# Kernel optimization log

Hardware: AMD Instinct MI355X
Metric: run time of the kernel (lower is better)

The kernel has to match this reference:

```python
import jax, jax.numpy as jnp
import numpy as np

BS = 64; T = 96; C = 16; IN = 16; H = 256; NH = 8; DH = H // NH
NCLS = 4; L = T + NCLS; LAYERS = 4; GDEP = 2; EPS = 1e-5


def _ln(x, g, b):
    m = x.mean(-1, keepdims=True)
    v = ((x - m) ** 2).mean(-1, keepdims=True)
    return (x - m) / jnp.sqrt(v + EPS) * g + b


def _mask():
    # causal upper-triangular -inf mask; last NCLS rows (cls tokens) attend everywhere
    m = jnp.where(jnp.triu(jnp.ones((L, L), jnp.float32), 1) > 0, -jnp.inf, 0.0)
    return m.at[-NCLS:].set(0.0)


def _enc(h, mask, Wqkv, bqkv, Wo, bo, W1, b1, W2, b2, g1, be1, g2, be2):
    # post-norm TransformerEncoderLayer (torch default), dropout=0
    B = h.shape[0]
    qkv = h @ Wqkv.T + bqkv
    q, k, v = jnp.split(qkv, 3, axis=-1)
    sp = lambda t: t.reshape(B, L, NH, DH).transpose(0, 2, 1, 3)
    q, k, v = sp(q), sp(k), sp(v)
    s = jnp.einsum('bhqd,bhkd->bhqk', q, k) / np.float32(np.sqrt(DH)) + mask
    a = jax.nn.softmax(s, axis=-1)
    o = jnp.einsum('bhqk,bhkd->bhqd', a, v).transpose(0, 2, 1, 3).reshape(B, L, H)
    h = _ln(h + o @ Wo.T + bo, g1, be1)
    ff = jax.nn.relu(h @ W1.T + b1) @ W2.T + b2
    return _ln(h + ff, g2, be2)


def _mixprop(x, g, Wm, bm):
    # x: (bs, H, C, NCLS); MTGNN mixprop with alpha=0
    adj = g + jnp.eye(C, dtype=g.dtype)
    a = adj / adj.sum(1, keepdims=True)
    h = x
    outs = [x]
    for _ in range(GDEP):
        h = jnp.einsum('ncwl,vw->ncvl', h, a)
        outs.append(h)
    ho = jnp.concatenate(outs, axis=1)  # (bs, (GDEP+1)*H, C, NCLS)
    return jnp.einsum('ncwl,oc->nowl', ho, Wm) + bm[None, :, None, None]


def _forward(x, Wfc, bfc, cls_token, pos_emb, emb1, emb2, Wl1, bl1, Wl2, bl2,
             Wqkv, bqkv, Wo, bo, W1, b1, W2, b2, ln1g, ln1b, ln2g, ln2b,
             Wmlp, bmlp, Wd1, bd1, Wd2, bd2):
    bs = x.shape[0]
    h = x @ Wfc.T + bfc                                      # (bs,T,C,H)
    h = jnp.concatenate([h, jnp.broadcast_to(cls_token, (bs, NCLS, C, H))], axis=1)
    h = h + pos_emb[None]                                    # (bs,L,C,H)
    h = jnp.swapaxes(h, 1, 2).reshape(bs * C, L, H)
    mask = _mask()
    # graph_constructor (alpha=1)
    m1 = jnp.tanh(emb1 @ Wl1.T + bl1)
    m2 = jnp.tanh(emb2 @ Wl2.T + bl2)
    g = jax.nn.relu(jnp.tanh(m1 @ m2.T - m2 @ m1.T))         # (C,C)
    h = _enc(h, mask, Wqkv[0], bqkv[0], Wo[0], bo[0], W1[0], b1[0], W2[0], b2[0],
             ln1g[0], ln1b[0], ln2g[0], ln2b[0])
    for l in range(1, LAYERS):
        cls = h[:, -NCLS:].reshape(bs, C, NCLS, H).transpose(0, 3, 1, 2)  # (bs,H,C,NCLS)
        cls = _mixprop(cls, g, Wmlp[l - 1], bmlp[l - 1])
        cls = cls.transpose(0, 2, 3, 1).reshape(bs * C, NCLS, H)
        h = jnp.concatenate([h[:, :-NCLS], cls], axis=1)
        h = _enc(h, mask, Wqkv[l], bqkv[l], Wo[l], bo[l], W1[l], b1[l], W2[l], b2[l],
                 ln1g[l], ln1b[l], ln2g[l], ln2b[l])
    z = jnp.tanh(h[:, -NCLS:].reshape(bs, C * NCLS * H))
    z = jax.nn.gelu(z @ Wd1.T + bd1, approximate=False) @ Wd2.T + bd2
    return z[:, 0]


def setup_inputs() -> dict:
    key = jax.random.key(0)
    ks = iter(jax.random.split(key, 64))
    rn = lambda *s: jax.random.normal(next(ks), s, dtype=jnp.float32) * 0.05
    d = {}
    d['x'] = jax.random.normal(next(ks), (BS, T, C, IN), dtype=jnp.float32)
    d['p'] = jnp.zeros((BS,), jnp.float32)
    d['y'] = jnp.zeros((BS,), jnp.float32)
    d['Wfc'] = rn(H, IN); d['bfc'] = jnp.zeros((H,), jnp.float32)
    d['cls_token'] = rn(1, NCLS, C, H) * 20.0  # torch randn scale ~1
    d['pos_emb'] = rn(NCLS + T, C, H) * 20.0
    d['emb1'] = rn(C, H); d['emb2'] = rn(C, H)
    d['Wl1'] = rn(H, H); d['bl1'] = jnp.zeros((H,), jnp.float32)
    d['Wl2'] = rn(H, H); d['bl2'] = jnp.zeros((H,), jnp.float32)
    d['Wqkv'] = rn(LAYERS, 3 * H, H); d['bqkv'] = jnp.zeros((LAYERS, 3 * H), jnp.float32)
    d['Wo'] = rn(LAYERS, H, H); d['bo'] = jnp.zeros((LAYERS, H), jnp.float32)
    d['W1'] = rn(LAYERS, 4 * H, H); d['b1'] = jnp.zeros((LAYERS, 4 * H), jnp.float32)
    d['W2'] = rn(LAYERS, H, 4 * H); d['b2'] = jnp.zeros((LAYERS, H), jnp.float32)
    d['ln1g'] = jnp.ones((LAYERS, H), jnp.float32); d['ln1b'] = jnp.zeros((LAYERS, H), jnp.float32)
    d['ln2g'] = jnp.ones((LAYERS, H), jnp.float32); d['ln2b'] = jnp.zeros((LAYERS, H), jnp.float32)
    d['Wmlp'] = rn(LAYERS - 1, H, (GDEP + 1) * H); d['bmlp'] = jnp.zeros((LAYERS - 1, H), jnp.float32)
    d['Wd1'] = rn(H, NCLS * C * H); d['bd1'] = jnp.zeros((H,), jnp.float32)
    d['Wd2'] = rn(1, H); d['bd2'] = jnp.zeros((1,), jnp.float32)
    return d


def reference(x, p, y, Wfc, bfc, cls_token, pos_emb, emb1, emb2, Wl1, bl1, Wl2, bl2,
              Wqkv, bqkv, Wo, bo, W1, b1, W2, b2, ln1g, ln1b, ln2g, ln2b,
              Wmlp, bmlp, Wd1, bd1, Wd2, bd2):
    # p, y are unused by the original forward (kept for signature parity)
    return _forward(x, Wfc, bfc, cls_token, pos_emb, emb1, emb2, Wl1, bl1, Wl2, bl2,
                    Wqkv, bqkv, Wo, bo, W1, b1, W2, b2, ln1g, ln1b, ln2g, ln2b,
                    Wmlp, bmlp, Wd1, bd1, Wd2, bd2)
```

## Files before the change

kernel.cpp:

```cpp
#include <hip/hip_runtime.h>
#include <hip/hip_bf16.h>
#include <math.h>

typedef unsigned short u16;
typedef unsigned int   u32;
typedef __attribute__((ext_vector_type(8))) short short8;
typedef __attribute__((ext_vector_type(4))) float f32x4;

#define BSZ   64
#define TT    96
#define CCH   16
#define INDIM 16
#define HD    256
#define NHEAD 8
#define DHEAD 32
#define NCLS  4
#define LSEQ  100
#define NLAY  4
#define EPSV  1e-5f
#define BSEQ  (BSZ*CCH)
#define MTOK  (BSEQ*LSEQ)

__device__ __forceinline__ float bf2f(u16 x){ return __uint_as_float(((u32)x)<<16); }
__device__ __forceinline__ u16 f2bf(float f){
    u32 u = __float_as_uint(f);
    u32 r = (u + 0x7fffu + ((u>>16)&1u)) >> 16;
    return (u16)r;
}
__device__ __forceinline__ float lo16(u32 r){ return __uint_as_float(r<<16); }
__device__ __forceinline__ float hi16(u32 r){ return __uint_as_float(r&0xffff0000u); }

__device__ __forceinline__ void gload_lds16(const u16* g, u16* l){
    __builtin_amdgcn_global_load_lds(
        (const __attribute__((address_space(1))) unsigned int*)g,
        (__attribute__((address_space(3))) unsigned int*)l, 16, 0, 0);
}

__global__ __launch_bounds__(256)
void k_cvt(const float* __restrict__ src, u16* __restrict__ dst, int n)
{
    for (int i = blockIdx.x*256 + threadIdx.x; i < n; i += gridDim.x*256)
        dst[i] = f2bf(src[i]);
}

__global__ __launch_bounds__(256)
void k_embed(const float* __restrict__ x, const float* __restrict__ Wfc,
             const float* __restrict__ bfc, const float* __restrict__ cls,
             const float* __restrict__ pos, u16* __restrict__ h)
{
    int s = blockIdx.x;
    int n = s >> 4, c = s & 15;
    int hc = threadIdx.x;
    float wr[INDIM];
    #pragma unroll
    for (int i=0;i<INDIM;i++) wr[i] = Wfc[hc*INDIM + i];
    float bb = bfc[hc];
    for (int l=0; l<TT; l++){
        const float* xr = x + (size_t)((n*TT + l)*CCH + c)*INDIM;
        float acc = bb;
        #pragma unroll
        for (int i=0;i<INDIM;i++) acc += xr[i]*wr[i];
        acc += pos[(size_t)(l*CCH + c)*HD + hc];
        h[((size_t)s*LSEQ + l)*HD + hc] = f2bf(acc);
    }
    #pragma unroll
    for (int l=TT; l<LSEQ; l++){
        float v = cls[(size_t)((l-TT)*CCH + c)*HD + hc]
                + pos[(size_t)(l*CCH + c)*HD + hc];
        h[((size_t)s*LSEQ + l)*HD + hc] = f2bf(v);
    }
}

__global__ __launch_bounds__(256)
void k_graph_m(const float* __restrict__ emb, const float* __restrict__ Wl,
               const float* __restrict__ bl, float* __restrict__ m)
{
    int r = blockIdx.x, o = threadIdx.x;
    __shared__ float e[HD];
    e[o] = emb[r*HD + o];
    __syncthreads();
    const float* w = Wl + (size_t)o*HD;
    float acc = bl[o];
    for (int k=0;k<HD;k++) acc += e[k]*w[k];
    m[r*HD + o] = tanhf(acc);
}

__global__ __launch_bounds__(256)
void k_graph_a(const float* __restrict__ m1, const float* __restrict__ m2,
               float* __restrict__ a)
{
    int t = threadIdx.x; int v = t >> 4, w = t & 15;
    __shared__ float adj[16][17];
    float s1=0.f, s2=0.f;
    for (int k=0;k<HD;k++){
        s1 += m1[v*HD+k]*m2[w*HD+k];
        s2 += m2[v*HD+k]*m1[w*HD+k];
    }
    float g = tanhf(s1 - s2); g = g > 0.f ? g : 0.f;
    adj[v][w] = g + (v==w ? 1.f : 0.f);
    __syncthreads();
    float rs = 0.f;
    #pragma unroll
    for (int j=0;j<16;j++) rs += adj[v][j];
    a[t] = adj[v][w] / rs;
}

__global__ __launch_bounds__(256)
void k_gemmA(const u16* __restrict__ A, int lda,
             const u16* __restrict__ W, const float* __restrict__ bias,
             u16* __restrict__ C, int ldc, int K, int relu, int scat)
{
    __shared__ u16 As0[128*32], As1[128*32];
    __shared__ u16 Ws0[128*32], Ws1[128*32];
    int t = threadIdx.x;
    int lane = t & 63, w = t >> 6;
    int wm = (w & 1)*64, wn = (w >> 1)*64;
    int fr = lane & 15, quad = lane >> 4;
    size_t mb = (size_t)blockIdx.x * 128;
    int nb = blockIdx.y * 128;
    int srow = lane >> 2;
    int sslot = lane & 3;

    f32x4 acc[4][4] = {};
    for (int k0 = 0; k0 < K; k0 += 64){
        __syncthreads();
        #pragma unroll
        for (int i=0;i<2;i++){
            int r = w*32 + i*16 + srow;
            int cw = sslot ^ ((r>>1)&3);
            gload_lds16(&A[(mb + r)*(size_t)lda + k0      + cw*8], &As0[(w*32 + i*16)*32]);
            gload_lds16(&A[(mb + r)*(size_t)lda + k0 + 32 + cw*8], &As1[(w*32 + i*16)*32]);
            gload_lds16(&W[(size_t)(nb + r)*K   + k0      + cw*8], &Ws0[(w*32 + i*16)*32]);
            gload_lds16(&W[(size_t)(nb + r)*K   + k0 + 32 + cw*8], &Ws1[(w*32 + i*16)*32]);
        }
        __syncthreads();
        short8 af0[4], af1[4], bf0[4], bf1[4];
        #pragma unroll
        for (int mt=0; mt<4; mt++){
            int r = wm + mt*16 + fr;
            int sw = (quad ^ ((r>>1)&3)) << 3;
            af0[mt] = *(const short8*)&As0[r*32 + sw];
            af1[mt] = *(const short8*)&As1[r*32 + sw];
        }
        #pragma unroll
        for (int nt=0; nt<4; nt++){
            int r = wn + nt*16 + fr;
            int sw = (quad ^ ((r>>1)&3)) << 3;
            bf0[nt] = *(const short8*)&Ws0[r*32 + sw];
            bf1[nt] = *(const short8*)&Ws1[r*32 + sw];
        }
        #pragma unroll
        for (int mt=0; mt<4; mt++)
            #pragma unroll
            for (int nt=0; nt<4; nt++){
                acc[mt][nt] = __builtin_amdgcn_mfma_f32_16x16x32_bf16(
                    af0[mt], bf0[nt], acc[mt][nt], 0, 0, 0);
                acc[mt][nt] = __builtin_amdgcn_mfma_f32_16x16x32_bf16(
                    af1[mt], bf1[nt], acc[mt][nt], 0, 0, 0);
            }
    }
    float bb[4];
    #pragma unroll
    for (int nt=0; nt<4; nt++) bb[nt] = bias[nb + wn + nt*16 + fr];
    #pragma unroll
    for (int mt=0; mt<4; mt++){
        #pragma unroll
        for (int nt=0; nt<4; nt++){
            #pragma unroll
            for (int r=0; r<4; r++){
                float v = acc[mt][nt][r] + bb[nt];
                if (relu) v = v > 0.f ? v : 0.f;
                size_t rg = mb + wm + mt*16 + quad*4 + r;
                if (scat) rg = (rg >> 2)*LSEQ + TT + (rg & 3);
                C[rg*(size_t)ldc + nb + wn + nt*16 + fr] = f2bf(v);
            }
        }
    }
}

__global__ __launch_bounds__(256)
void k_gemmC(const u16* __restrict__ A, int lda, int K,
             const u16* __restrict__ W, const float* __restrict__ bias,
             u16* __restrict__ h, const float* __restrict__ gam,
             const float* __restrict__ bet, size_t row0)
{
    __shared__ u16 As0[64*32], As1[64*32];
    __shared__ u16 Ws0[256*32], Ws1[256*32];
    int t = threadIdx.x;
    int lane = t & 63, w = t >> 6;
    int fr = lane & 15, quad = lane >> 4;
    size_t mb = (size_t)blockIdx.x * 64;
    int srow = lane >> 2, sslot = lane & 3;

    f32x4 acc[4][4] = {};
    for (int k0 = 0; k0 < K; k0 += 64){
        __syncthreads();
        {
            int r = w*16 + srow;
            int cw = sslot ^ ((r>>1)&3);
            gload_lds16(&A[(mb + r)*(size_t)lda + k0      + cw*8], &As0[(w*16)*32]);
            gload_lds16(&A[(mb + r)*(size_t)lda + k0 + 32 + cw*8], &As1[(w*16)*32]);
        }
        #pragma unroll
        for (int i=0;i<4;i++){
            int r = w*64 + i*16 + srow;
            int cw = sslot ^ ((r>>1)&3);
            gload_lds16(&W[(size_t)r*K + k0      + cw*8], &Ws0[(w*64 + i*16)*32]);
            gload_lds16(&W[(size_t)r*K + k0 + 32 + cw*8], &Ws1[(w*64 + i*16)*32]);
        }
        __syncthreads();
        short8 af0[4], af1[4], bf0[4], bf1[4];
        #pragma unroll
        for (int mt=0; mt<4; mt++){
            int ra = mt*16 + fr;
            int swa = (quad ^ ((ra>>1)&3)) << 3;
            af0[mt] = *(const short8*)&As0[ra*32 + swa];
            af1[mt] = *(const short8*)&As1[ra*32 + swa];
        }
        #pragma unroll
        for (int nt=0; nt<4; nt++){
            int rb = w*64 + nt*16 + fr;
            int swb = (quad ^ ((rb>>1)&3)) << 3;
            bf0[nt] = *(const short8*)&Ws0[rb*32 + swb];
            bf1[nt] = *(const short8*)&Ws1[rb*32 + swb];
        }
        #pragma unroll
        for (int mt=0; mt<4; mt++)
            #pragma unroll
            for (int nt=0; nt<4; nt++){
                acc[mt][nt] = __builtin_amdgcn_mfma_f32_16x16x32_bf16(
                    af0[mt], bf0[nt], acc[mt][nt], 0, 0, 0);
                acc[mt][nt] = __builtin_amdgcn_mfma_f32_16x16x32_bf16(
                    af1[mt], bf1[nt], acc[mt][nt], 0, 0, 0);
            }
    }

    float bb[4], gg[4], be[4];
    #pragma unroll
    for (int nt=0; nt<4; nt++){
        int col = w*64 + nt*16 + fr;
        bb[nt] = bias[col]; gg[nt] = gam[col]; be[nt] = bet[col];
    }
    #pragma unroll
    for (int mt=0; mt<4; mt++){
        #pragma unroll
        for (int r=0; r<4; r++){
            size_t row = row0 + mb + mt*16 + quad*4 + r;
            #pragma unroll
            for (int nt=0; nt<4; nt++)
                acc[mt][nt][r] += bb[nt] + bf2f(h[row*HD + w*64 + nt*16 + fr]);
        }
    }
    __syncthreads();
    float* red  = (float*)As0;
    float* red2 = (float*)As1;
    float ps[4][4];
    #pragma unroll
    for (int mt=0; mt<4; mt++)
        #pragma unroll
        for (int r=0; r<4; r++){
            float s = acc[mt][0][r] + acc[mt][1][r] + acc[mt][2][r] + acc[mt][3][r];
            s += __shfl_xor(s,1,64); s += __shfl_xor(s,2,64);
            s += __shfl_xor(s,4,64); s += __shfl_xor(s,8,64);
            ps[mt][r] = s;
        }
    if (fr == 0){
        #pragma unroll
        for (int mt=0; mt<4; mt++)
            #pragma unroll
            for (int r=0; r<4; r++)
                red[w*64 + mt*16 + quad*4 + r] = ps[mt][r];
    }
    __syncthreads();
    float mean[4][4];
    #pragma unroll
    for (int mt=0; mt<4; mt++)
        #pragma unroll
        for (int r=0; r<4; r++){
            int rl = mt*16 + quad*4 + r;
            mean[mt][r] = (red[rl] + red[64+rl] + red[128+rl] + red[192+rl]) * (1.f/256.f);
            float s = 0.f;
            #pragma unroll
            for (int nt=0; nt<4; nt++){ float d = acc[mt][nt][r] - mean[mt][r]; s += d*d; }
            s += __shfl_xor(s,1,64); s += __shfl_xor(s,2,64);
            s += __shfl_xor(s,4,64); s += __shfl_xor(s,8,64);
            ps[mt][r] = s;
        }
    if (fr == 0){
        #pragma unroll
        for (int mt=0; mt<4; mt++)
            #pragma unroll
            for (int r=0; r<4; r++)
                red2[w*64 + mt*16 + quad*4 + r] = ps[mt][r];
    }
    __syncthreads();
    #pragma unroll
    for (int mt=0; mt<4; mt++)
        #pragma unroll
        for (int r=0; r<4; r++){
            int rl = mt*16 + quad*4 + r;
            float inv = rsqrtf((red2[rl] + red2[64+rl] + red2[128+rl] + red2[192+rl])
                               * (1.f/256.f) + EPSV);
            size_t row = row0 + mb + rl;
            #pragma unroll
            for (int nt=0; nt<4; nt++)
                h[row*HD + w*64 + nt*16 + fr] =
                    f2bf((acc[mt][nt][r] - mean[mt][r]) * inv * gg[nt] + be[nt]);
        }
}

#define KS_STR 40
#define VT_STR 136
#define PL_STR 136
__global__ __launch_bounds__(256)
void k_attn(u16* __restrict__ qkv)
{
    __shared__ u16 smem[26368];
    int t = threadIdx.x;
    int w = t >> 6, lane = t & 63;
    int fr = lane & 15, quad = lane >> 4;
    int p = t >> 7, t2 = t & 127;
    u16* Ks = smem + p*4480;
    u16* Vt = smem + 8960 + p*4352;
    u16* Pl = smem + 17664 + w*2176;

    {
        int gp = blockIdx.x*2 + p;
        size_t base = (size_t)(gp >> 3)*LSEQ*768 + (gp & 7)*32;
        for (int idx = t2; idx < 1792; idx += 128){
            int key = idx >> 4, d2 = (idx & 15) << 1;
            u32 kv = (key < LSEQ) ? *(const u32*)&qkv[base + (size_t)key*768 + 256 + d2] : 0u;
            *(u32*)&Ks[key*KS_STR + d2] = kv;
        }
        for (int idx = t2; idx < 2048; idx += 128){
            int key = idx >> 4, d2 = (idx & 15) << 1;
            u32 vv = (key < LSEQ) ? *(const u32*)&qkv[base + (size_t)key*768 + 512 + d2] : 0u;
            Vt[ d2   *VT_STR + key] = (u16)(vv & 0xffffu);
            Vt[(d2+1)*VT_STR + key] = (u16)(vv >> 16);
        }
    }
    __syncthreads();

    int wp = w >> 1;
    int gp = blockIdx.x*2 + wp;
    size_t base = (size_t)(gp >> 3)*LSEQ*768 + (gp & 7)*32;
    u16* Ksw = smem + wp*4480;
    u16* Vtw = smem + 8960 + wp*4352;

    short8 kf[7];
    #pragma unroll
    for (int nt=0; nt<7; nt++)
        kf[nt] = *(const short8*)&Ksw[(nt*16 + fr)*KS_STR + quad*8];
    short8 vfr[4][2];
    #pragma unroll
    for (int ks=0; ks<4; ks++)
        #pragma unroll
        for (int nt=0; nt<2; nt++)
            vfr[ks][nt] = *(const short8*)&Vtw[(nt*16 + fr)*VT_STR + ks*32 + quad*8];

    const float scale = 0.17677669529663687f;
    int smask = (w & 1) ? 0x34 : 0x4B;
    #pragma unroll
    for (int st = 0; st < 7; ++st){
        if (!((smask >> st) & 1)) continue;
        const int ntile = (st == 6) ? 7 : (st + 1);
        const int nks   = (st == 6) ? 4 : (st/2 + 1);
        int q = st*16 + fr;
        short8 qf = {};
        if (q < LSEQ) qf = *(const short8*)&qkv[base + (size_t)q*768 + quad*8];
        f32x4 S[7];
        #pragma unroll
        for (int nt=0; nt<7; nt++){
            if (nt >= ntile) continue;
            f32x4 z = {};
            S[nt] = __builtin_amdgcn_mfma_f32_16x16x32_bf16(qf, kf[nt], z, 0,0,0);
        }
        float mx[4] = {-1e30f,-1e30f,-1e30f,-1e30f};
        #pragma unroll
        for (int r=0;r<4;r++){
            int qr = st*16 + quad*4 + r;
            int jmax = (qr < TT) ? qr : (LSEQ-1);
            #pragma unroll
            for (int nt=0;nt<7;nt++){
                if (nt >= ntile) continue;
                int j = nt*16 + fr;
                float s = (j <= jmax) ? S[nt][r]*scale : -1e30f;
                S[nt][r] = s;
                mx[r] = fmaxf(mx[r], s);
            }
        }
        #pragma unroll
        for (int r=0;r<4;r++){
            #pragma unroll
            for (int m=1;m<16;m<<=1) mx[r] = fmaxf(mx[r], __shfl_xor(mx[r], m, 64));
        }
        float l4[4] = {0.f,0.f,0.f,0.f};
        #pragma unroll
        for (int r=0;r<4;r++){
            #pragma unroll
            for (int nt=0;nt<7;nt++){
                if (nt >= ntile) continue;
                float pv = __expf(S[nt][r] - mx[r]);
                S[nt][r] = pv;
                l4[r] += pv;
            }
        }
        #pragma unroll
        for (int r=0;r<4;r++){
            #pragma unroll
            for (int m=1;m<16;m<<=1) l4[r] += __shfl_xor(l4[r], m, 64);
        }
        #pragma unroll
        for (int nt=0;nt<7;nt++){
            if (nt >= ntile) continue;
            #pragma unroll
            for (int r=0;r<4;r++){
                u16 hb = f2bf(S[nt][r]);
                Pl[(quad*4+r)*PL_STR + nt*16 + fr] = hb;
                S[nt][r] -= bf2f(hb);
            }
        }
        if (ntile*16 < nks*32){
            #pragma unroll
            for (int r=0;r<4;r++)
                Pl[(quad*4+r)*PL_STR + ntile*16 + fr] = 0;
        }
        __builtin_amdgcn_s_waitcnt(0);
        f32x4 D[2] = {};
        #pragma unroll
        for (int ks=0; ks<4; ks++){
            if (ks >= nks) continue;
            short8 pf = *(const short8*)&Pl[fr*PL_STR + ks*32 + quad*8];
            #pragma unroll
            for (int nt=0; nt<2; nt++)
                D[nt] = __builtin_amdgcn_mfma_f32_16x16x32_bf16(pf, vfr[ks][nt], D[nt], 0,0,0);
        }
        __builtin_amdgcn_s_waitcnt(0);
        #pragma unroll
        for (int nt=0;nt<7;nt++){
            if (nt >= ntile) continue;
            #pragma unroll
            for (int r=0;r<4;r++)
                Pl[(quad*4+r)*PL_STR + nt*16 + fr] = f2bf(S[nt][r]);
        }
        __builtin_amdgcn_s_waitcnt(0);
        #pragma unroll
        for (int ks=0; ks<4; ks++){
            if (ks >= nks) continue;
            short8 pf = *(const short8*)&Pl[fr*PL_STR + ks*32 + quad*8];
            #pragma unroll
            for (int nt=0; nt<2; nt++)
                D[nt] = __builtin_amdgcn_mfma_f32_16x16x32_bf16(pf, vfr[ks][nt], D[nt], 0,0,0);
        }
        #pragma unroll
        for (int r=0;r<4;r++){
            int qr = st*16 + quad*4 + r;
            if (qr < LSEQ){
                float inv = 1.f / l4[r];
                #pragma unroll
                for (int nt=0; nt<2; nt++)
                    qkv[base + (size_t)qr*768 + nt*16 + fr] = f2bf(D[nt][r]*inv);
            }
        }
        __builtin_amdgcn_s_waitcnt(0);
    }
}

__global__ __launch_bounds__(256)
void k_mixprep(const u16* __restrict__ h, const float* __restrict__ a,
               u16* __restrict__ amid)
{
    int n = blockIdx.x >> 2, tt = blockIdx.x & 3;
    __shared__ float xs[256][17], h1s[256][17], h2s[256][17];
    __shared__ float as[16][17];
    int t = threadIdx.x;
    as[t>>4][t&15] = a[t];
    for (int idx=t; idx<4096; idx+=256){
        int w = idx >> 8, hc = idx & 255;
        xs[hc][w] = bf2f(h[((size_t)(n*16 + w)*LSEQ + TT + tt)*HD + hc]);
    }
    __syncthreads();
    for (int idx=t; idx<4096; idx+=256){
        int v = idx & 15, hc = idx >> 4;
        float acc = 0.f;
        #pragma unroll
        for (int w=0;w<16;w++) acc += as[v][w]*xs[hc][w];
        h1s[hc][v] = acc;
    }
    __syncthreads();
    for (int idx=t; idx<4096; idx+=256){
        int v = idx & 15, hc = idx >> 4;
        float acc = 0.f;
        #pragma unroll
        for (int w=0;w<16;w++) acc += as[v][w]*h1s[hc][w];
        h2s[hc][v] = acc;
    }
    __syncthreads();
    int hc = t;
    #pragma unroll
    for (int w=0;w<16;w++){
        size_t row = (size_t)((n*16 + w)*4 + tt);
        amid[row*768 +       hc] = f2bf(xs[hc][w]);
        amid[row*768 + 256 + hc] = f2bf(h1s[hc][w]);
        amid[row*768 + 512 + hc] = f2bf(h2s[hc][w]);
    }
}

__global__ __launch_bounds__(256)
void k_z(const u16* __restrict__ h, u16* __restrict__ z)
{
    int bid = blockIdx.x, t = threadIdx.x;
    #pragma unroll
    for (int tc=0;tc<4;tc++)
        z[((size_t)bid*4 + tc)*HD + t] = f2bf(tanhf(bf2f(h[((size_t)bid*LSEQ + TT + tc)*HD + t])));
}

__global__ __launch_bounds__(256)
void k_head1p(const u16* __restrict__ z, const float* __restrict__ Wd1,
              float* __restrict__ d1p)
{
    __shared__ float zch[64][137];
    __shared__ float wt[16][137];
    int t = threadIdx.x;
    int col = t & 15, rgrp = t >> 4;
    int ob = blockIdx.x * 16;
    int kb = blockIdx.y;
    float acc[4] = {0.f,0.f,0.f,0.f};
    for (int kc=0; kc<1024; kc+=128){
        int base_k = kb*1024 + kc;
        #pragma unroll
        for (int jj=0; jj<16; jj++){
            int idx = t + jj*256;
            int n = idx >> 6, k2 = (idx & 63) << 1;
            u32 r = *(const u32*)&z[(size_t)n*16384 + base_k + k2];
            zch[n][k2] = lo16(r); zch[n][k2+1] = hi16(r);
        }
        #pragma unroll
        for (int jj=0; jj<2; jj++){
            int idx = t + jj*256;
            int r = idx >> 5, k4 = (idx & 31) << 2;
            float4 w4 = *(const float4*)&Wd1[(size_t)(ob + r)*16384 + base_k + k4];
            wt[r][k4] = w4.x; wt[r][k4+1] = w4.y; wt[r][k4+2] = w4.z; wt[r][k4+3] = w4.w;
        }
        __syncthreads();
        for (int k=0;k<128;k++){
            float wv = wt[col][k];
            #pragma unroll
            for (int u=0;u<4;u++) acc[u] += zch[rgrp + 16*u][k]*wv;
        }
        __syncthreads();
    }
    #pragma unroll
    for (int u=0;u<4;u++)
        d1p[(size_t)(kb*64 + rgrp + 16*u)*HD + ob + col] = acc[u];
}

__global__ __launch_bounds__(256)
void k_headf(const float* __restrict__ d1p, const float* __restrict__ bd1,
             const float* __restrict__ Wd2, const float* __restrict__ bd2,
             float* __restrict__ out)
{
    __shared__ float red[4];
    int n = blockIdx.x, c = threadIdx.x;
    float s = 0.f;
    #pragma unroll
    for (int kb=0; kb<16; kb++) s += d1p[(size_t)(kb*64 + n)*HD + c];
    float xx = s + bd1[c];
    float ge = 0.5f*xx*(1.f + erff(xx*0.70710678118654752f));
    float p = ge * Wd2[c];
    #pragma unroll
    for (int m=1;m<64;m<<=1) p += __shfl_xor(p, m, 64);
    if ((c & 63) == 0) red[c >> 6] = p;
    __syncthreads();
    if (c == 0) out[n] = red[0]+red[1]+red[2]+red[3] + bd2[0];
}

extern "C" void kernel_launch(void* const* d_in, const int* in_sizes, int n_in,
                              void* d_out, int out_size, void* d_ws, size_t ws_size,
                              hipStream_t stream)
{
    const float* x    = (const float*)d_in[0];
    const float* Wfc  = (const float*)d_in[3];
    const float* bfc  = (const float*)d_in[4];
    const float* cls  = (const float*)d_in[5];
    const float* pos  = (const float*)d_in[6];
    const float* emb1 = (const float*)d_in[7];
    const float* emb2 = (const float*)d_in[8];
    const float* Wl1  = (const float*)d_in[9];
    const float* bl1  = (const float*)d_in[10];
    const float* Wl2  = (const float*)d_in[11];
    const float* bl2  = (const float*)d_in[12];
    const float* Wqkv = (const float*)d_in[13];
    const float* bqkv = (const float*)d_in[14];
    const float* Wo   = (const float*)d_in[15];
    const float* bo   = (const float*)d_in[16];
    const float* W1   = (const float*)d_in[17];
    const float* b1   = (const float*)d_in[18];
    const float* W2   = (const float*)d_in[19];
    const float* b2   = (const float*)d_in[20];
    const float* ln1g = (const float*)d_in[21];
    const float* ln1b = (const float*)d_in[22];
    const float* ln2g = (const float*)d_in[23];
    const float* ln2b = (const float*)d_in[24];
    const float* Wmlp = (const float*)d_in[25];
    const float* bmlp = (const float*)d_in[26];
    const float* Wd1  = (const float*)d_in[27];
    const float* bd1  = (const float*)d_in[28];
    const float* Wd2  = (const float*)d_in[29];
    const float* bd2  = (const float*)d_in[30];

    int NCH = 8;
    {
        const size_t fixed = 63145088 + (1<<20);
        if      (fixed + (size_t)MTOK    *2560 <= ws_size) NCH = 1;
        else if (fixed + (size_t)(MTOK/2)*2560 <= ws_size) NCH = 2;
        else if (fixed + (size_t)(MTOK/4)*2560 <= ws_size) NCH = 4;
    }
    const int RCH = MTOK / NCH;
    const int SCH = BSEQ / NCH;

    u16* h    = (u16*)d_ws;
    u16* buf  = h    + (size_t)MTOK*HD;
    u16* buf2 = buf  + (size_t)RCH*1024;
    u16* wq   = buf2 + (size_t)RCH*256;
    u16* wo   = wq   + (size_t)4*768*256;
    u16* w1   = wo   + (size_t)4*256*256;
    u16* w2   = w1   + (size_t)4*1024*256;
    u16* wmb  = w2   + (size_t)4*256*1024;
    u16* zb   = wmb  + (size_t)3*256*768;
    float* fp = (float*)(zb + (size_t)BSZ*16384);
    float* m1  = fp;
    float* m2  = m1 + CCH*HD;
    float* an  = m2 + CCH*HD;
    float* d1p = an + CCH*CCH;

    k_cvt<<<512, 256, 0, stream>>>(Wqkv, wq, 4*768*256);
    k_cvt<<<256, 256, 0, stream>>>(Wo,   wo, 4*256*256);
    k_cvt<<<512, 256, 0, stream>>>(W1,   w1, 4*1024*256);
    k_cvt<<<512, 256, 0, stream>>>(W2,   w2, 4*256*1024);
    k_cvt<<<256, 256, 0, stream>>>(Wmlp, wmb, 3*256*768);

    k_embed<<<BSEQ, 256, 0, stream>>>(x, Wfc, bfc, cls, pos, h);
    k_graph_m<<<16, 256, 0, stream>>>(emb1, Wl1, bl1, m1);
    k_graph_m<<<16, 256, 0, stream>>>(emb2, Wl2, bl2, m2);
    k_graph_a<<<1, 256, 0, stream>>>(m1, m2, an);

    for (int l=0; l<NLAY; l++){
        if (l > 0){
            k_mixprep<<<BSZ*NCLS, 256, 0, stream>>>(h, an, buf);
            k_gemmA<<<dim3(4096/128, 256/128), 256, 0, stream>>>(
                buf, 768, wmb + (size_t)(l-1)*256*768, bmlp + (size_t)(l-1)*HD,
                h, HD, 768, 0, 1);
        }

        for (int c=0; c<NCH; c++){
            size_t row0 = (size_t)c * RCH;
            k_gemmA<<<dim3(RCH/128, 768/128), 256, 0, stream>>>(
                h + row0*HD, HD, wq + (size_t)l*768*256, bqkv + (size_t)l*768,
                buf, 768, HD, 0, 0);
            k_attn<<<SCH*NHEAD/2, 256, 0, stream>>>(buf);
            k_gemmC<<<RCH/64, 256, 0, stream>>>(
                buf, 768, HD, wo + (size_t)l*256*256, bo + (size_t)l*HD,
                h, ln1g + (size_t)l*HD, ln1b + (size_t)l*HD, row0);
            k_gemmA<<<dim3(RCH/128, 1024/128), 256, 0, stream>>>(
                h + row0*HD, HD, w1 + (size_t)l*1024*256, b1 + (size_t)l*1024,
                buf, 1024, HD, 1, 0);
            k_gemmC<<<RCH/64, 256, 0, stream>>>(
                buf, 1024, 1024, w2 + (size_t)l*256*1024, b2 + (size_t)l*HD,
                h, ln2g + (size_t)l*HD, ln2b + (size_t)l*HD, row0);
        }
    }

    k_z<<<BSZ*CCH, 256, 0, stream>>>(h, zb);
    k_head1p<<<dim3(16, 16), 256, 0, stream>>>(zb, Wd1, d1p);
    k_headf<<<BSZ, 256, 0, stream>>>(d1p, bd1, Wd2, bd2, (float*)d_out);
}
```

Baseline: 2.352 ms.

## Double-buffer LDS tiles in GEMM kernels and use packed bf16 conversion

Both GEMM kernels get two LDS buffers. The next K-tile's global-to-LDS loads are issued before computing the current tile, with one waitcnt and barrier per step, so memory latency overlaps the MFMA work. The epilogues replace the software bf16 rounding with the v_cvt_pk_bf16_f32 instruction. Doubling LDS use (k_gemmC goes to about 80KB) can lower occupancy and limit how many blocks fit per CU.

```diff
diff --git a/kernel.cpp b/kernel.cpp
--- a/kernel.cpp
+++ b/kernel.cpp
@@ -30,6 +30,12 @@
 __device__ __forceinline__ float lo16(u32 r){ return __uint_as_float(r<<16); }
 __device__ __forceinline__ float hi16(u32 r){ return __uint_as_float(r&0xffff0000u); }
 
+__device__ __forceinline__ u32 cvtpk(float lo, float hi){
+    u32 r;
+    asm("v_cvt_pk_bf16_f32 %0, %1, %2" : "=v"(r) : "v"(lo), "v"(hi));
+    return r;
+}
+
 __device__ __forceinline__ void gload_lds16(const u16* g, u16* l){
     __builtin_amdgcn_global_load_lds(
         (const __attribute__((address_space(1))) unsigned int*)g,
@@ -110,8 +116,8 @@
              const u16* __restrict__ W, const float* __restrict__ bias,
              u16* __restrict__ C, int ldc, int K, int relu, int scat)
 {
-    __shared__ u16 As0[128*32], As1[128*32];
-    __shared__ u16 Ws0[128*32], Ws1[128*32];
+    __shared__ u16 As0[2][128*32], As1[2][128*32];
+    __shared__ u16 Ws0[2][128*32], Ws1[2][128*32];
     int t = threadIdx.x;
     int lane = t & 63, w = t >> 6;
     int wm = (w & 1)*64, wn = (w >> 1)*64;
@@ -122,32 +128,33 @@
     int sslot = lane & 3;
 
     f32x4 acc[4][4] = {};
-    for (int k0 = 0; k0 < K; k0 += 64){
-        __syncthreads();
+
+    auto STAGE = [&](int bb, int k0){
         #pragma unroll
         for (int i=0;i<2;i++){
             int r = w*32 + i*16 + srow;
             int cw = sslot ^ ((r>>1)&3);
-            gload_lds16(&A[(mb + r)*(size_t)lda + k0      + cw*8], &As0[(w*32 + i*16)*32]);
-            gload_lds16(&A[(mb + r)*(size_t)lda + k0 + 32 + cw*8], &As1[(w*32 + i*16)*32]);
-            gload_lds16(&W[(size_t)(nb + r)*K   + k0      + cw*8], &Ws0[(w*32 + i*16)*32]);
-            gload_lds16(&W[(size_t)(nb + r)*K   + k0 + 32 + cw*8], &Ws1[(w*32 + i*16)*32]);
-        }
-        __syncthreads();
+            gload_lds16(&A[(mb + r)*(size_t)lda + k0      + cw*8], &As0[bb][(w*32 + i*16)*32]);
+            gload_lds16(&A[(mb + r)*(size_t)lda + k0 + 32 + cw*8], &As1[bb][(w*32 + i*16)*32]);
+            gload_lds16(&W[(size_t)(nb + r)*K   + k0      + cw*8], &Ws0[bb][(w*32 + i*16)*32]);
+            gload_lds16(&W[(size_t)(nb + r)*K   + k0 + 32 + cw*8], &Ws1[bb][(w*32 + i*16)*32]);
+        }
+    };
+    auto COMPUTE = [&](int bb){
         short8 af0[4], af1[4], bf0[4], bf1[4];
         #pragma unroll
         for (int mt=0; mt<4; mt++){
             int r = wm + mt*16 + fr;
             int sw = (quad ^ ((r>>1)&3)) << 3;
-            af0[mt] = *(const short8*)&As0[r*32 + sw];
-            af1[mt] = *(const short8*)&As1[r*32 + sw];
+            af0[mt] = *(const short8*)&As0[bb][r*32 + sw];
+            af1[mt] = *(const short8*)&As1[bb][r*32 + sw];
         }
         #pragma unroll
         for (int nt=0; nt<4; nt++){
             int r = wn + nt*16 + fr;
             int sw = (quad ^ ((r>>1)&3)) << 3;
-            bf0[nt] = *(const short8*)&Ws0[r*32 + sw];
-            bf1[nt] = *(const short8*)&Ws1[r*32 + sw];
+            bf0[nt] = *(const short8*)&Ws0[bb][r*32 + sw];
+            bf1[nt] = *(const short8*)&Ws1[bb][r*32 + sw];
         }
         #pragma unroll
         for (int mt=0; mt<4; mt++)
@@ -158,22 +165,50 @@
                 acc[mt][nt] = __builtin_amdgcn_mfma_f32_16x16x32_bf16(
                     af1[mt], bf1[nt], acc[mt][nt], 0, 0, 0);
             }
-    }
-    float bb[4];
-    #pragma unroll
-    for (int nt=0; nt<4; nt++) bb[nt] = bias[nb + wn + nt*16 + fr];
+    };
+
+    const int nst = K >> 6;
+    STAGE(0, 0);
+    asm volatile("s_waitcnt vmcnt(0)" ::: "memory");
+    __builtin_amdgcn_s_barrier();
+    int b = 0;
+    for (int ts = 0; ts < nst; ++ts){
+        if (ts + 1 < nst) STAGE(b^1, (ts+1) << 6);
+        COMPUTE(b);
+        asm volatile("s_waitcnt vmcnt(0)" ::: "memory");
+        __builtin_amdgcn_s_barrier();
+        b ^= 1;
+    }
+
+    float bb4[4];
+    #pragma unroll
+    for (int nt=0; nt<4; nt++) bb4[nt] = bias[nb + wn + nt*16 + fr];
     #pragma unroll
     for (int mt=0; mt<4; mt++){
+        size_t rbase = mb + wm + mt*16 + quad*4;
+        size_t rows[4];
+        #pragma unroll
+        for (int r=0; r<4; r++){
+            size_t rg = rbase + r;
+            if (scat) rg = (rg >> 2)*LSEQ + TT + (rg & 3);
+            rows[r] = rg*(size_t)ldc;
+        }
         #pragma unroll
         for (int nt=0; nt<4; nt++){
-            #pragma unroll
-            for (int r=0; r<4; r++){
-                float v = acc[mt][nt][r] + bb[nt];
-                if (relu) v = v > 0.f ? v : 0.f;
-                size_t rg = mb + wm + mt*16 + quad*4 + r;
-                if (scat) rg = (rg >> 2)*LSEQ + TT + (rg & 3);
-                C[rg*(size_t)ldc + nb + wn + nt*16 + fr] = f2bf(v);
+            int col = nb + wn + nt*16 + fr;
+            float v0 = acc[mt][nt][0] + bb4[nt];
+            float v1 = acc[mt][nt][1] + bb4[nt];
+            float v2 = acc[mt][nt][2] + bb4[nt];
+            float v3 = acc[mt][nt][3] + bb4[nt];
+            if (relu){
+                v0 = v0 > 0.f ? v0 : 0.f;  v1 = v1 > 0.f ? v1 : 0.f;
+                v2 = v2 > 0.f ? v2 : 0.f;  v3 = v3 > 0.f ? v3 : 0.f;
             }
+            u32 p01 = cvtpk(v0, v1), p23 = cvtpk(v2, v3);
+            C[rows[0] + col] = (u16)p01;
+            C[rows[1] + col] = (u16)(p01 >> 16);
+            C[rows[2] + col] = (u16)p23;
+            C[rows[3] + col] = (u16)(p23 >> 16);
         }
     }
 }
@@ -184,8 +219,8 @@
              u16* __restrict__ h, const float* __restrict__ gam,
              const float* __restrict__ bet, size_t row0)
 {
-    __shared__ u16 As0[64*32], As1[64*32];
-    __shared__ u16 Ws0[256*32], Ws1[256*32];
+    __shared__ u16 As0[2][64*32], As1[2][64*32];
+    __shared__ u16 Ws0[2][256*32], Ws1[2][256*32];
     int t = threadIdx.x;
     int lane = t & 63, w = t >> 6;
     int fr = lane & 15, quad = lane >> 4;
@@ -193,36 +228,37 @@
     int srow = lane >> 2, sslot = lane & 3;
 
     f32x4 acc[4][4] = {};
-    for (int k0 = 0; k0 < K; k0 += 64){
-        __syncthreads();
+
+    auto STAGE = [&](int bb, int k0){
         {
             int r = w*16 + srow;
             int cw = sslot ^ ((r>>1)&3);
-            gload_lds16(&A[(mb + r)*(size_t)lda + k0      + cw*8], &As0[(w*16)*32]);
-            gload_lds16(&A[(mb + r)*(size_t)lda + k0 + 32 + cw*8], &As1[(w*16)*32]);
+            gload_lds16(&A[(mb + r)*(size_t)lda + k0      + cw*8], &As0[bb][(w*16)*32]);
+            gload_lds16(&A[(mb + r)*(size_t)lda + k0 + 32 + cw*8], &As1[bb][(w*16)*32]);
         }
         #pragma unroll
         for (int i=0;i<4;i++){
             int r = w*64 + i*16 + srow;
             int cw = sslot ^ ((r>>1)&3);
-            gload_lds16(&W[(size_t)r*K + k0      + cw*8], &Ws0[(w*64 + i*16)*32]);
-            gload_lds16(&W[(size_t)r*K + k0 + 32 + cw*8], &Ws1[(w*64 + i*16)*32]);
-        }
-        __syncthreads();
+            gload_lds16(&W[(size_t)r*K + k0      + cw*8], &Ws0[bb][(w*64 + i*16)*32]);
+            gload_lds16(&W[(size_t)r*K + k0 + 32 + cw*8], &Ws1[bb][(w*64 + i*16)*32]);
+        }
+    };
+    auto COMPUTE = [&](int bb){
         short8 af0[4], af1[4], bf0[4], bf1[4];
         #pragma unroll
         for (int mt=0; mt<4; mt++){
             int ra = mt*16 + fr;
             int swa = (quad ^ ((ra>>1)&3)) << 3;
-            af0[mt] = *(const short8*)&As0[ra*32 + swa];
-            af1[mt] = *(const short8*)&As1[ra*32 + swa];
+            af0[mt] = *(const short8*)&As0[bb][ra*32 + swa];
+            af1[mt] = *(const short8*)&As1[bb][ra*32 + swa];
         }
         #pragma unroll
         for (int nt=0; nt<4; nt++){
             int rb = w*64 + nt*16 + fr;
             int swb = (quad ^ ((rb>>1)&3)) << 3;
-            bf0[nt] = *(const short8*)&Ws0[rb*32 + swb];
-            bf1[nt] = *(const short8*)&Ws1[rb*32 + swb];
+            bf0[nt] = *(const short8*)&Ws0[bb][rb*32 + swb];
+            bf1[nt] = *(const short8*)&Ws1[bb][rb*32 + swb];
         }
         #pragma unroll
         for (int mt=0; mt<4; mt++)
@@ -233,13 +269,26 @@
                 acc[mt][nt] = __builtin_amdgcn_mfma_f32_16x16x32_bf16(
                     af1[mt], bf1[nt], acc[mt][nt], 0, 0, 0);
             }
-    }
-
-    float bb[4], gg[4], be[4];
+    };
+
+    const int nst = K >> 6;
+    STAGE(0, 0);
+    asm volatile("s_waitcnt vmcnt(0)" ::: "memory");
+    __builtin_amdgcn_s_barrier();
+    int b = 0;
+    for (int ts = 0; ts < nst; ++ts){
+        if (ts + 1 < nst) STAGE(b^1, (ts+1) << 6);
+        COMPUTE(b);
+        asm volatile("s_waitcnt vmcnt(0)" ::: "memory");
+        __builtin_amdgcn_s_barrier();
+        b ^= 1;
+    }
+
+    float bb4[4], gg[4], be[4];
     #pragma unroll
     for (int nt=0; nt<4; nt++){
         int col = w*64 + nt*16 + fr;
-        bb[nt] = bias[col]; gg[nt] = gam[col]; be[nt] = bet[col];
+        bb4[nt] = bias[col]; gg[nt] = gam[col]; be[nt] = bet[col];
     }
     #pragma unroll
     for (int mt=0; mt<4; mt++){
@@ -248,7 +297,7 @@
             size_t row = row0 + mb + mt*16 + quad*4 + r;
             #pragma unroll
             for (int nt=0; nt<4; nt++)
-                acc[mt][nt][r] += bb[nt] + bf2f(h[row*HD + w*64 + nt*16 + fr]);
+                acc[mt][nt][r] += bb4[nt] + bf2f(h[row*HD + w*64 + nt*16 + fr]);
         }
     }
     __syncthreads();
@@ -302,10 +351,15 @@
             float inv = rsqrtf((red2[rl] + red2[64+rl] + red2[128+rl] + red2[192+rl])
                                * (1.f/256.f) + EPSV);
             size_t row = row0 + mb + rl;
-            #pragma unroll
-            for (int nt=0; nt<4; nt++)
-                h[row*HD + w*64 + nt*16 + fr] =
-                    f2bf((acc[mt][nt][r] - mean[mt][r]) * inv * gg[nt] + be[nt]);
+            float o0 = (acc[mt][0][r] - mean[mt][r]) * inv * gg[0] + be[0];
+            float o1 = (acc[mt][1][r] - mean[mt][r]) * inv * gg[1] + be[1];
+            float o2 = (acc[mt][2][r] - mean[mt][r]) * inv * gg[2] + be[2];
+            float o3 = (acc[mt][3][r] - mean[mt][r]) * inv * gg[3] + be[3];
+            u32 p01 = cvtpk(o0, o1), p23 = cvtpk(o2, o3);
+            h[row*HD + w*64 +  0 + fr] = (u16)p01;
+            h[row*HD + w*64 + 16 + fr] = (u16)(p01 >> 16);
+            h[row*HD + w*64 + 32 + fr] = (u16)p23;
+            h[row*HD + w*64 + 48 + fr] = (u16)(p23 >> 16);
         }
 }
 
```

Measured after the change: 2.257 ms. 1.04x faster.
